# Performance work log

Measured on AMD Instinct MI355X. Metric: run time of the kernel, lower is better.

The kernel has to match this reference:

```python
import jax, jax.numpy as jnp
import numpy as np

N_NODES = 100000
N_EDGES = 800000
NODE_F = 32
EDGE_F = 16
HID = 128
EPS = 1e-5


def _bn(h, g, b):
    # BatchNorm1d in training mode: biased batch stats over dim 0
    m = h.mean(axis=0)
    v = jnp.mean((h - m) ** 2, axis=0)
    return (h - m) * jax.lax.rsqrt(v + EPS) * g + b


def _sage(x, src, dst, Wl, bl, Wr):
    # PyG SAGEConv (mean aggr): lin_l(mean_{j->i} x_j) + lin_r(x_i)
    s = jax.ops.segment_sum(x[src], dst, num_segments=N_NODES)
    cnt = jax.ops.segment_sum(jnp.ones((src.shape[0], 1), x.dtype), dst, num_segments=N_NODES)
    mean = s / jnp.maximum(cnt, 1.0)
    return mean @ Wl + bl + x @ Wr


def setup_inputs() -> dict:
    key = jax.random.key(0)
    ks = jax.random.split(key, 32)

    def lin(k, fi, fo):
        return jax.random.normal(k, (fi, fo), jnp.float32) / np.sqrt(fi)

    inp = {
        'x': jax.random.normal(ks[0], (N_NODES, NODE_F), jnp.float32),
        'edge_index': jax.random.randint(ks[1], (2, N_EDGES), 0, N_NODES),
        'edge_attr': jax.random.normal(ks[2], (N_EDGES, EDGE_F), jnp.float32),
        'edge_source': jax.random.randint(ks[3], (N_EDGES,), 0, N_NODES),
        'edge_target': jax.random.randint(ks[4], (N_EDGES,), 0, N_NODES),
        'W1l': lin(ks[5], NODE_F, HID), 'b1': jnp.zeros((HID,), jnp.float32), 'W1r': lin(ks[6], NODE_F, HID),
        'W2l': lin(ks[7], HID, HID), 'b2': jnp.zeros((HID,), jnp.float32), 'W2r': lin(ks[8], HID, HID),
        'bn1_g': jnp.ones((HID,), jnp.float32), 'bn1_b': jnp.zeros((HID,), jnp.float32),
        'bn2_g': jnp.ones((HID,), jnp.float32), 'bn2_b': jnp.zeros((HID,), jnp.float32),
        'We': lin(ks[9], EDGE_F, HID), 'be': jnp.zeros((HID,), jnp.float32),
        'bne_g': jnp.ones((HID,), jnp.float32), 'bne_b': jnp.zeros((HID,), jnp.float32),
        'Wm1': lin(ks[10], 3 * HID, HID), 'bm1': jnp.zeros((HID,), jnp.float32),
        'bnm_g': jnp.ones((HID,), jnp.float32), 'bnm_b': jnp.zeros((HID,), jnp.float32),
        'Wm2': lin(ks[11], HID, HID // 2), 'bm2': jnp.zeros((HID // 2,), jnp.float32),
        'Wm3': lin(ks[12], HID // 2, 1), 'bm3': jnp.zeros((1,), jnp.float32),
    }
    return inp


def reference(x, edge_index, edge_attr, edge_source, edge_target,
              W1l, b1, W1r, W2l, b2, W2r, bn1_g, bn1_b, bn2_g, bn2_b,
              We, be, bne_g, bne_b, Wm1, bm1, bnm_g, bnm_b, Wm2, bm2, Wm3, bm3):
    src, dst = edge_index[0], edge_index[1]
    h = jax.nn.relu(_bn(_sage(x, src, dst, W1l, b1, W1r), bn1_g, bn1_b))  # dropout = identity (eval)
    h = jax.nn.relu(_bn(_sage(h, src, dst, W2l, b2, W2r), bn2_g, bn2_b))
    ef = _bn(jax.nn.relu(edge_attr @ We + be), bne_g, bne_b)  # Linear->ReLU->BN->Dropout(id)
    z = jnp.concatenate([h[edge_source], h[edge_target], ef], axis=1)  # [E, 3*HID]
    z = _bn(jax.nn.relu(z @ Wm1 + bm1), bnm_g, bnm_b)
    z = jax.nn.relu(z @ Wm2 + bm2)
    return (z @ Wm3 + bm3).squeeze(-1)
```

## Files before the change

kernel.cpp:

```cpp
#include <hip/hip_runtime.h>
#include <hip/hip_bf16.h>

#define NN 100000
#define NE 800000
#define SCAN_NB 98

typedef __attribute__((ext_vector_type(8))) short bf16x8;
typedef __attribute__((ext_vector_type(4))) float f32x4;

__device__ __forceinline__ short f2b(float f) {
    unsigned u = __float_as_uint(f);
    unsigned r = (u + 0x7fffu + ((u >> 16) & 1u)) >> 16;
    return (short)r;
}
__device__ __forceinline__ float b2f(short s) {
    return __uint_as_float(((unsigned)(unsigned short)s) << 16);
}

__global__ __launch_bounds__(256) void k_prep_hist(
    const float* __restrict__ We, const float* __restrict__ Wm1,
    const float* __restrict__ W2l, const float* __restrict__ W2r,
    short* __restrict__ WteT, short* __restrict__ WmsT,
    short* __restrict__ WmdT, short* __restrict__ W2cT,
    const int* __restrict__ ei, int* __restrict__ deg)
{
    int b = blockIdx.x;
    int tid = threadIdx.x;
    if (b >= 5) {
        int e = (b - 5) * 256 + tid;
        if (e < NE) atomicAdd(&deg[ei[NE + e]], 1);
        return;
    }
// ... 85 lines not shown
    }
    float s1[4] = {0,0,0,0}, s2[4] = {0,0,0,0};
    f32x4 zero = {0.f, 0.f, 0.f, 0.f};
    __syncthreads();

    const int G = gridDim.x - SCAT_NB;
    const int NT = NE / 32;
    float4 fe0 = {0,0,0,0}, fe1 = {0,0,0,0};
    int t = blockIdx.x - SCAT_NB;
    if (t < NT && quad < 2) {
        const float* p = ea + (size_t)(t * 32 + row16 + ln) * 16 + quad * 8;
        fe0 = *(const float4*)p; fe1 = *(const float4*)(p + 4);
    }
    for (; t < NT; t += G) {
        bf16x8 aE;
        #pragma unroll
        for (int i = 0; i < 8; i++) aE[i] = 0;
        if (quad < 2) {
            aE[0]=f2b(fe0.x); aE[1]=f2b(fe0.y); aE[2]=f2b(fe0.z); aE[3]=f2b(fe0.w);
            aE[4]=f2b(fe1.x); aE[5]=f2b(fe1.y); aE[6]=f2b(fe1.z); aE[7]=f2b(fe1.w);
        }
        int t1 = t + G;
        if (t1 < NT && quad < 2) {
            const float* p = ea + (size_t)(t1 * 32 + row16 + ln) * 16 + quad * 8;
            fe0 = *(const float4*)p; fe1 = *(const float4*)(p + 4);
        }
        f32x4 tacc[4];
        #pragma unroll
        for (int nt = 0; nt < 4; nt++)
            tacc[nt] = __builtin_amdgcn_mfma_f32_16x16x32_bf16(aE, bWe[nt], zero, 0, 0, 0);
        #pragma unroll
        for (int nt = 0; nt < 4; nt++)
            #pragma unroll
            for (int r = 0; r < 4; r++) {
                float v = fmaxf(tacc[nt][r] + bec[nt], 0.f);
// ... 73 lines not shown
    int c0 = (threadIdx.x & 31) * 4;
    float sc[4], sh[4];
    #pragma unroll
    for (int i = 0; i < 4; i++) {
        float m = ssum1[c0 + i] / (float)NN;
        float var = ssq1[c0 + i] / (float)NN - m * m;
        float rs = rsqrtf(var + 1e-5f);
        float s = g1[c0 + i] * rs;
        sc[i] = s; sh[i] = b1g[c0 + i] - m * s;
    }
    int b = rowptr[n], e = rowptr[n + 1];
    float acc[4] = {0.f, 0.f, 0.f, 0.f};
    int i = b;
    for (; i + 4 <= e; i += 4) {
        int s0 = elist[i], s1 = elist[i + 1], s2 = elist[i + 2], s3 = elist[i + 3];
        ushort4 u0 = *(const ushort4*)(h1b + (size_t)s0 * 128 + c0);
        ushort4 u1 = *(const ushort4*)(h1b + (size_t)s1 * 128 + c0);
        ushort4 u2 = *(const ushort4*)(h1b + (size_t)s2 * 128 + c0);
        ushort4 u3 = *(const ushort4*)(h1b + (size_t)s3 * 128 + c0);
        acc[0] += fmaxf(b2f((short)u0.x) * sc[0] + sh[0], 0.f) + fmaxf(b2f((short)u1.x) * sc[0] + sh[0], 0.f)
                + fmaxf(b2f((short)u2.x) * sc[0] + sh[0], 0.f) + fmaxf(b2f((short)u3.x) * sc[0] + sh[0], 0.f);
        acc[1] += fmaxf(b2f((short)u0.y) * sc[1] + sh[1], 0.f) + fmaxf(b2f((short)u1.y) * sc[1] + sh[1], 0.f)
                + fmaxf(b2f((short)u2.y) * sc[1] + sh[1], 0.f) + fmaxf(b2f((short)u3.y) * sc[1] + sh[1], 0.f);
        acc[2] += fmaxf(b2f((short)u0.z) * sc[2] + sh[2], 0.f) + fmaxf(b2f((short)u1.z) * sc[2] + sh[2], 0.f)
                + fmaxf(b2f((short)u2.z) * sc[2] + sh[2], 0.f) + fmaxf(b2f((short)u3.z) * sc[2] + sh[2], 0.f);
        acc[3] += fmaxf(b2f((short)u0.w) * sc[3] + sh[3], 0.f) + fmaxf(b2f((short)u1.w) * sc[3] + sh[3], 0.f)
                + fmaxf(b2f((short)u2.w) * sc[3] + sh[3], 0.f) + fmaxf(b2f((short)u3.w) * sc[3] + sh[3], 0.f);
    }
    for (; i < e; i++) {
        int s = elist[i];
        ushort4 u = *(const ushort4*)(h1b + (size_t)s * 128 + c0);
        acc[0] += fmaxf(b2f((short)u.x) * sc[0] + sh[0], 0.f);
        acc[1] += fmaxf(b2f((short)u.y) * sc[1] + sh[1], 0.f);
        acc[2] += fmaxf(b2f((short)u.z) * sc[2] + sh[2], 0.f);
        acc[3] += fmaxf(b2f((short)u.w) * sc[3] + sh[3], 0.f);
    }
    float inv = (e > b) ? 1.0f / (float)(e - b) : 1.0f;
    ushort4 o;
    o.x = (unsigned short)f2b(acc[0] * inv);
    o.y = (unsigned short)f2b(acc[1] * inv);
    o.z = (unsigned short)f2b(acc[2] * inv);
    o.w = (unsigned short)f2b(acc[3] * inv);
    *(ushort4*)(m2b + (size_t)n * 128 + c0) = o;
}

__global__ __launch_bounds__(256) void k_node_l1(
    const float* __restrict__ meanX, const float* __restrict__ x,
    const float* __restrict__ Wl, const float* __restrict__ Wr,
    const float* __restrict__ bias,
    short* __restrict__ outp, float* __restrict__ ssum, float* __restrict__ ssq)
{
    __shared__ __align__(16) float sWl[32][128];
    __shared__ __align__(16) float sWr[32][128];
    __shared__ __align__(16) float sA[32][36];
    __shared__ __align__(16) float sB[32][36];
    __shared__ float red[2][128], red2[2][128];
    int tid = threadIdx.x;
    int j = tid & 127, rg = tid >> 7;
// ... 18 lines not shown
    for (int kq = 0; kq < 8; kq++) {
        int k = kq * 4;
        float wl0 = sWl[k][j], wl1 = sWl[k+1][j], wl2 = sWl[k+2][j], wl3 = sWl[k+3][j];
        float wr0 = sWr[k][j], wr1 = sWr[k+1][j], wr2 = sWr[k+2][j], wr3 = sWr[k+3][j];
        #pragma unroll
        for (int r = 0; r < 16; r++) {
            float4 a = *(float4*)(&sA[rb + r][k]);
            float4 b = *(float4*)(&sB[rb + r][k]);
            acc[r] += a.x*wl0 + a.y*wl1 + a.z*wl2 + a.w*wl3
                    + b.x*wr0 + b.y*wr1 + b.z*wr2 + b.w*wr3;
        }
    }
    float bj = bias[j];
    float s1 = 0.0f, s2 = 0.0f;
    #pragma unroll
    for (int r = 0; r < 16; r++) {
        float v = acc[r] + bj;
        outp[(size_t)(r0 + rb + r) * 128 + j] = f2b(v);
        s1 += v; s2 += v * v;
    }
    red[rg][j] = s1; red2[rg][j] = s2;
    __syncthreads();
    if (rg == 0) {
        atomicAdd(&ssum[j], red[0][j] + red[1][j]);
        atomicAdd(&ssq[j],  red2[0][j] + red2[1][j]);
    }
}

__global__ __launch_bounds__(256) void k_node_l2m(
    const short* __restrict__ m2b, const short* __restrict__ h1b,
    const float* __restrict__ ssum1, const float* __restrict__ ssq1,
    const float* __restrict__ g1, const float* __restrict__ b1g,
    const short* __restrict__ W2cT, const float* __restrict__ bias,
    short* __restrict__ h2b, float* __restrict__ ssum, float* __restrict__ ssq)
// ... 27 lines not shown
    float s1[4] = {0,0,0,0}, s2[4] = {0,0,0,0};
    f32x4 zero = {0.f, 0.f, 0.f, 0.f};
    __syncthreads();

    for (int t = blockIdx.x; t < NN / 32; t += gridDim.x) {
        int r0 = t * 32;
        __syncthreads();
        {
            int r = tid >> 3, seg = tid & 7;
            if (seg < 4) {
                const bf16x8* src = (const bf16x8*)(m2b + (size_t)(r0 + r) * 128 + seg * 32);
                bf16x8* dst = (bf16x8*)(&sK[r][seg * 32]);
                dst[0] = src[0]; dst[1] = src[1]; dst[2] = src[2]; dst[3] = src[3];
            } else {
                int c0 = (seg - 4) * 32;
                const short* src = h1b + (size_t)(r0 + r) * 128 + c0;
                short tmp[32];
                #pragma unroll
                for (int i = 0; i < 32; i++)
                    tmp[i] = f2b(fmaxf(b2f(src[i]) * sS[c0 + i] + sH[c0 + i], 0.f));
                bf16x8* dst = (bf16x8*)(&sK[r][128 + c0]);
                dst[0] = *(bf16x8*)(tmp); dst[1] = *(bf16x8*)(tmp + 8);
                dst[2] = *(bf16x8*)(tmp + 16); dst[3] = *(bf16x8*)(tmp + 24);
            }
        }
        __syncthreads();
        f32x4 acc[4] = {zero, zero, zero, zero};
        #pragma unroll
        for (int kk = 0; kk < 8; kk++) {
            bf16x8 a = *(const bf16x8*)(&sK[row16 + ln][kk * 32 + quad * 8]);
            #pragma unroll
            for (int nt = 0; nt < 4; nt++)
                acc[nt] = __builtin_amdgcn_mfma_f32_16x16x32_bf16(a, bW[nt][kk], acc[nt], 0, 0, 0);
        }
        #pragma unroll
        for (int nt = 0; nt < 4; nt++) {
            int col = colbase + nt * 16 + ln;
            #pragma unroll
            for (int r = 0; r < 4; r++) {
                float v = acc[nt][r] + bc[nt];
                h2b[(size_t)(r0 + row16 + quad * 4 + r) * 128 + col] = f2b(v);
                s1[nt] += v; s2[nt] += v * v;
            }
        }
    }
    #pragma unroll
    for (int nt = 0; nt < 4; nt++) {
        float a1 = s1[nt], a2 = s2[nt];
        a1 += __shfl_down(a1, 32); a1 += __shfl_down(a1, 16);
        a2 += __shfl_down(a2, 32); a2 += __shfl_down(a2, 16);
        if (quad == 0) {
            atomicAdd(&sRed[0][colbase + nt * 16 + ln], a1);
            atomicAdd(&sRed[1][colbase + nt * 16 + ln], a2);
        }
    }
    __syncthreads();
    if (tid < 128) {
        atomicAdd(&ssum[tid], sRed[0][tid]);
        atomicAdd(&ssq[tid],  sRed[1][tid]);
    }
}

__global__ void k_fold_m(const float* __restrict__ ssum, const float* __restrict__ ssq,
    const float* __restrict__ g, const float* __restrict__ b,
    const float* __restrict__ Wm2, const float* __restrict__ bm2,
    short* __restrict__ W2pT, float* __restrict__ b2p)
{
    __shared__ float sa[128], sc[128];
    int tid = threadIdx.x;
    float m = ssum[tid] / (float)NE;
    float var = ssq[tid] / (float)NE - m * m;
    float rs = rsqrtf(var + 1e-5f);
    float a = g[tid] * rs;
    sa[tid] = a; sc[tid] = b[tid] - m * a;
    __syncthreads();
    if (tid < 64) {
        float acc = bm2[tid];
        for (int k = 0; k < 128; k++) {
            float w = Wm2[k * 64 + tid];
            W2pT[tid * 128 + k] = f2b(sa[k] * w);
            acc += sc[k] * w;
        }
        b2p[tid] = acc;
    }
}

__global__ __launch_bounds__(256) void k_proj_mfma(
    const short* __restrict__ h2b,
    const float* __restrict__ ssum2, const float* __restrict__ ssq2,
    const float* __restrict__ g2, const float* __restrict__ b2g,
    const short* __restrict__ WT0, const short* __restrict__ WT1,
    short* __restrict__ C0, short* __restrict__ C1)
{
    __shared__ __align__(16) short sA[32][136];
    __shared__ float sS[128], sH[128];
    const int tid = threadIdx.x;
    const int wave = tid >> 6, lane = tid & 63, quad = lane >> 4, ln = lane & 15;
    const int waveM = wave >> 1, waveN = wave & 1;
// ... 10 lines not shown
        sS[tid] = s; sH[tid] = b2g[tid] - m * s;
    }
    bf16x8 bW[4][4];
    #pragma unroll
    for (int nt = 0; nt < 4; nt++)
        #pragma unroll
        for (int kk = 0; kk < 4; kk++)
            bW[nt][kk] = *(const bf16x8*)(WT + (colbase + nt * 16 + ln) * 128 + kk * 32 + quad * 8);
    f32x4 zero = {0.f, 0.f, 0.f, 0.f};
    __syncthreads();
    for (int t = b0; t < NN / 32; t += 512) {
        int r0 = t * 32;
        __syncthreads();
        {
            int r = tid >> 3, c0 = (tid & 7) * 16;
            const short* p = h2b + (size_t)(r0 + r) * 128 + c0;
            short tmp[16];
            #pragma unroll
            for (int i = 0; i < 16; i++)
                tmp[i] = f2b(fmaxf(b2f(p[i]) * sS[c0 + i] + sH[c0 + i], 0.f));
            *(bf16x8*)(&sA[r][c0])     = *(bf16x8*)tmp;
            *(bf16x8*)(&sA[r][c0 + 8]) = *(bf16x8*)(tmp + 8);
        }
        __syncthreads();
        f32x4 acc[4] = {zero, zero, zero, zero};
        #pragma unroll
        for (int kk = 0; kk < 4; kk++) {
            bf16x8 a = *(const bf16x8*)(&sA[row16 + ln][kk * 32 + quad * 8]);
            #pragma unroll
            for (int nt = 0; nt < 4; nt++)
                acc[nt] = __builtin_amdgcn_mfma_f32_16x16x32_bf16(a, bW[nt][kk], acc[nt], 0, 0, 0);
        }
        #pragma unroll
        for (int nt = 0; nt < 4; nt++) {
            int col = colbase + nt * 16 + ln;
            #pragma unroll
            for (int r = 0; r < 4; r++)
                C[(size_t)(r0 + row16 + quad * 4 + r) * 128 + col] = f2b(acc[nt][r]);
        }
    }
}

template<int MODE, bool STOREV = false>
__global__ __launch_bounds__(256) void k_edge_mfma(
    const float* __restrict__ ea,
    const short* __restrict__ WteT, const float* __restrict__ be,
    const short* __restrict__ W1pT, const float* __restrict__ bm1p,
    const short* __restrict__ hs, const short* __restrict__ hd,
    const int* __restrict__ esrc, const int* __restrict__ etgt,
    const short* __restrict__ W2pT, const float* __restrict__ b2p,
    const float* __restrict__ Wm3, const float* __restrict__ bm3,
    float* __restrict__ ssum, float* __restrict__ ssq,
    short* __restrict__ vbuf, float* __restrict__ outp)
{
    __shared__ __align__(16) short sT[32][136];
    __shared__ __align__(16) float sSum[32][132];
    __shared__ float sRed[2][128];
    __shared__ __align__(16) short sWe[128][16];
    __shared__ __align__(16) short sW2[64][136];
    __shared__ float sZ[32][69];
    __shared__ float sW3[64];

    const int tid = threadIdx.x;
    const int wave = tid >> 6, lane = tid & 63;
    const int quad = lane >> 4, ln = lane & 15;
    const int waveM = wave >> 1, waveN = wave & 1;
    const int colbase = 64 * waveN, row16 = 16 * waveM;

    if (MODE < 2) {
        if (tid < 128) { sRed[0][tid] = 0.f; sRed[1][tid] = 0.f; }
    }
    if (MODE <= 2) {
        int r = tid >> 1, cs = (tid & 1) * 8;
        *(bf16x8*)(&sWe[r][cs]) = *(const bf16x8*)(WteT + r * 32 + cs);
    }
    if (MODE >= 2) {
        int q = tid >> 2, kb = (tid & 3) * 32;
        const bf16x8* src = (const bf16x8*)(W2pT + q * 128 + kb);
        bf16x8* dst = (bf16x8*)(&sW2[q][kb]);
        dst[0] = src[0]; dst[1] = src[1]; dst[2] = src[2]; dst[3] = src[3];
        if (tid < 64) sW3[tid] = Wm3[tid];
    }

    bf16x8 bW1[4][4];
    if (MODE == 1 || MODE == 2) {
        #pragma unroll
        for (int nt = 0; nt < 4; nt++)
            #pragma unroll
            for (int kk = 0; kk < 4; kk++)
                bW1[nt][kk] = *(const bf16x8*)(W1pT + (colbase + nt * 16 + ln) * 128 + kk * 32 + quad * 8);
    }
    float bec[4], bmc[4];
    #pragma unroll
    for (int nt = 0; nt < 4; nt++) {
        bec[nt] = (MODE <= 2) ? be[colbase + nt * 16 + ln] : 0.f;
        bmc[nt] = (MODE == 1 || MODE == 2) ? bm1p[colbase + nt * 16 + ln] : 0.f;
    }
    float b2c[2] = {0.f, 0.f};
    if (MODE >= 2) { b2c[0] = b2p[32 * waveN + ln]; b2c[1] = b2p[32 * waveN + 16 + ln]; }
    float bm3v = (MODE >= 2) ? bm3[0] : 0.f;

    const int srow = tid >> 4;
    const int scol = (tid & 15) * 8;

    float s1[4] = {0,0,0,0}, s2[4] = {0,0,0,0};
    f32x4 zero = {0.f, 0.f, 0.f, 0.f};
    __syncthreads();

    if constexpr (MODE == 1) {
        const int G = gridDim.x;
        const int NT = NE / 32;
        bf16x8 gA = {}, gB = {}, gC = {}, gD = {};
        int i1sA = 0, i1tA = 0, i1sB = 0, i1tB = 0;
        float4 fe0 = {0,0,0,0}, fe1 = {0,0,0,0};
// ... 11 lines not shown
            if (t1 < NT) {
                const int e1 = t1 * 32;
                i1sA = esrc[e1 + srow];      i1tA = etgt[e1 + srow];
                i1sB = esrc[e1 + srow + 16]; i1tB = etgt[e1 + srow + 16];
            }
            if (quad < 2) {
                const float* p = ea + (size_t)(e0 + row16 + ln) * 16 + quad * 8;
                fe0 = *(const float4*)p; fe1 = *(const float4*)(p + 4);
            }
        }

        for (; t < NT; t += G) {
            const int e0 = t * 32;

            bf16x8 aE;
            #pragma unroll
            for (int i = 0; i < 8; i++) aE[i] = 0;
            if (quad < 2) {
                aE[0]=f2b(fe0.x); aE[1]=f2b(fe0.y); aE[2]=f2b(fe0.z); aE[3]=f2b(fe0.w);
                aE[4]=f2b(fe1.x); aE[5]=f2b(fe1.y); aE[6]=f2b(fe1.z); aE[7]=f2b(fe1.w);
            }
            f32x4 tacc[4];
            #pragma unroll
            for (int nt = 0; nt < 4; nt++) {
                bf16x8 bWe_ = *(const bf16x8*)(&sWe[colbase + nt * 16 + ln][(quad & 1) * 8]);
                tacc[nt] = __builtin_amdgcn_mfma_f32_16x16x32_bf16(aE, bWe_, zero, 0, 0, 0);
            }

            __syncthreads();

            #pragma unroll
            for (int nt = 0; nt < 4; nt++) {
                int col = colbase + nt * 16 + ln;
                #pragma unroll
                for (int r = 0; r < 4; r++)
                    sT[row16 + quad * 4 + r][col] = f2b(fmaxf(tacc[nt][r] + bec[nt], 0.f));
            }
            {
                f32x4 a0, a1, b0, b1;
                #pragma unroll
                for (int i = 0; i < 4; i++) {
                    a0[i] = b2f(gA[i])     + b2f(gB[i]);
                    a1[i] = b2f(gA[i + 4]) + b2f(gB[i + 4]);
                    b0[i] = b2f(gC[i])     + b2f(gD[i]);
                    b1[i] = b2f(gC[i + 4]) + b2f(gD[i + 4]);
                }
                *(f32x4*)(&sSum[srow][scol])          = a0;
                *(f32x4*)(&sSum[srow][scol + 4])      = a1;
                *(f32x4*)(&sSum[srow + 16][scol])     = b0;
                *(f32x4*)(&sSum[srow + 16][scol + 4]) = b1;
            }
            {
                int t1 = t + G;
                if (t1 < NT) {
                    gA = *(const bf16x8*)(hs + (size_t)i1sA * 128 + scol);
                    gB = *(const bf16x8*)(hd + (size_t)i1tA * 128 + scol);
                    gC = *(const bf16x8*)(hs + (size_t)i1sB * 128 + scol);
                    gD = *(const bf16x8*)(hd + (size_t)i1tB * 128 + scol);
                    int t2 = t1 + G;
                    if (t2 < NT) {
                        const int e2 = t2 * 32;
// ... 7 lines not shown
                }
            }
            __syncthreads();

            f32x4 uacc[4] = {zero, zero, zero, zero};
            #pragma unroll
            for (int kk = 0; kk < 4; kk++) {
                bf16x8 aU = *(const bf16x8*)(&sT[row16 + ln][kk * 32 + quad * 8]);
                #pragma unroll
                for (int nt = 0; nt < 4; nt++)
                    uacc[nt] = __builtin_amdgcn_mfma_f32_16x16x32_bf16(aU, bW1[nt][kk], uacc[nt], 0, 0, 0);
            }
            #pragma unroll
            for (int nt = 0; nt < 4; nt++) {
                int col = colbase + nt * 16 + ln;
                #pragma unroll
                for (int r = 0; r < 4; r++) {
                    float v = uacc[nt][r] + bmc[nt] + sSum[row16 + quad * 4 + r][col];
                    v = fmaxf(v, 0.f);
                    s1[nt] += v; s2[nt] += v * v;
                    if constexpr (STOREV)
                        vbuf[(size_t)(e0 + row16 + quad * 4 + r) * 128 + col] = f2b(v);
                }
            }
        }
    } else if constexpr (MODE == 3) {
        const int G = gridDim.x;
        const int NT = NE / 32;
        bf16x8 aV0 = {}, aV1 = {}, aV2 = {}, aV3 = {};
        int t = blockIdx.x;
        if (t < NT) {
            const short* p = vbuf + (size_t)(t * 32 + row16 + ln) * 128 + quad * 8;
            aV0 = *(const bf16x8*)(p);
            aV1 = *(const bf16x8*)(p + 32);
            aV2 = *(const bf16x8*)(p + 64);
            aV3 = *(const bf16x8*)(p + 96);
        }
// ... 31 lines not shown
            }
            __syncthreads();
            {
                int row = wave * 8 + (lane >> 3);
                int ks  = (lane & 7) * 8;
                float o = 0.f;
                #pragma unroll
                for (int k2 = 0; k2 < 8; k2++)
                    o += sZ[row][ks + k2] * sW3[ks + k2];
                o += __shfl_xor(o, 1);
                o += __shfl_xor(o, 2);
                o += __shfl_xor(o, 4);
                if ((lane & 7) == 0) outp[e0 + row] = o + bm3v;
            }
        }
    } else {
    for (int t = blockIdx.x; t < NE / 32; t += gridDim.x) {
        const int e0 = t * 32;

        int isA = esrc[e0 + srow],      itA = etgt[e0 + srow];
        int isB = esrc[e0 + srow + 16], itB = etgt[e0 + srow + 16];

        bf16x8 aE;
        #pragma unroll
        for (int i = 0; i < 8; i++) aE[i] = 0;
        if (quad < 2) {
            const float* p = ea + (size_t)(e0 + row16 + ln) * 16 + quad * 8;
            float4 f0 = *(const float4*)p, f1 = *(const float4*)(p + 4);
            aE[0]=f2b(f0.x); aE[1]=f2b(f0.y); aE[2]=f2b(f0.z); aE[3]=f2b(f0.w);
            aE[4]=f2b(f1.x); aE[5]=f2b(f1.y); aE[6]=f2b(f1.z); aE[7]=f2b(f1.w);
        }
        f32x4 tacc[4];
        #pragma unroll
        for (int nt = 0; nt < 4; nt++) {
            bf16x8 bWe_ = *(const bf16x8*)(&sWe[colbase + nt * 16 + ln][(quad & 1) * 8]);
            tacc[nt] = __builtin_amdgcn_mfma_f32_16x16x32_bf16(aE, bWe_, zero, 0, 0, 0);
        }

        __syncthreads();
        {
            bf16x8 gA = *(const bf16x8*)(hs + (size_t)isA * 128 + scol);
            bf16x8 gB = *(const bf16x8*)(hd + (size_t)itA * 128 + scol);
            bf16x8 gC = *(const bf16x8*)(hs + (size_t)isB * 128 + scol);
            bf16x8 gD = *(const bf16x8*)(hd + (size_t)itB * 128 + scol);
            #pragma unroll
            for (int nt = 0; nt < 4; nt++) {
                int col = colbase + nt * 16 + ln;
                #pragma unroll
                for (int r = 0; r < 4; r++)
                    sT[row16 + quad * 4 + r][col] = f2b(fmaxf(tacc[nt][r] + bec[nt], 0.f));
            }
            f32x4 a0, a1, b0, b1;
            #pragma unroll
            for (int i = 0; i < 4; i++) {
                a0[i] = b2f(gA[i])     + b2f(gB[i]);
                a1[i] = b2f(gA[i + 4]) + b2f(gB[i + 4]);
                b0[i] = b2f(gC[i])     + b2f(gD[i]);
                b1[i] = b2f(gC[i + 4]) + b2f(gD[i + 4]);
            }
            *(f32x4*)(&sSum[srow][scol])          = a0;
            *(f32x4*)(&sSum[srow][scol + 4])      = a1;
            *(f32x4*)(&sSum[srow + 16][scol])     = b0;
            *(f32x4*)(&sSum[srow + 16][scol + 4]) = b1;
        }
        __syncthreads();

        f32x4 uacc[4] = {zero, zero, zero, zero};
        #pragma unroll
        for (int kk = 0; kk < 4; kk++) {
            bf16x8 aU = *(const bf16x8*)(&sT[row16 + ln][kk * 32 + quad * 8]);
            #pragma unroll
            for (int nt = 0; nt < 4; nt++)
                uacc[nt] = __builtin_amdgcn_mfma_f32_16x16x32_bf16(aU, bW1[nt][kk], uacc[nt], 0, 0, 0);
        }
// ... 100 lines not shown
    float* bm1p  = (float*)A(512); float* b2p = (float*)A(256);
    short* WteT  = (short*)A(128 * 32 * 2);
    short* W1pT  = (short*)A(128 * 128 * 2);
    short* WmsT  = (short*)A(128 * 128 * 2);
    short* WmdT  = (short*)A(128 * 128 * 2);
    short* W2pT  = (short*)A(64 * 128 * 2);
    short* W2cT  = (short*)A(128 * 256 * 2);
    size_t chain = o;
    float* meanX = (float*)A((size_t)NN * 32 * 4);
    short* h1b   = (short*)A((size_t)NN * 128 * 2);
    short* m2b   = (short*)A((size_t)NN * 128 * 2);
    short* h2b   = (short*)A((size_t)NN * 128 * 2);
    int*   stmp  = (int*)meanX;
    short* vbuf  = (short*)(base + chain);
    bool storev = ws_size >= chain + (size_t)NE * 128 * 2;

    hipMemsetAsync(deg, 0, (size_t)NN * 4, stream);
    hipMemsetAsync(st, 0, 1024 * 4, stream);

    k_prep_hist<<<5 + (NE + 255) / 256, 256, 0, stream>>>(We, Wm1, W2l, W2r,
        WteT, WmsT, WmdT, W2cT, ei, deg);
    k_scan_a<<<SCAN_NB, 1024, 0, stream>>>(deg, stmp, bsum);
    k_scan_b<<<1, 64, 0, stream>>>(bsum, boff, rowptr);
    k_scan_c<<<SCAN_NB, 1024, 0, stream>>>(stmp, boff, rowptr, wp);

    k_scat_e0<<<SCAT_NB + 2048, 256, 0, stream>>>(ei, wp, elist,
        eattr, WteT, be, st + 512, st + 640);

    k_gagg1f<<<NN / 8 + 1, 256, 0, stream>>>(x, rowptr, elist, meanX,
        st + 512, st + 640, bne_g, bne_b, Wm1, bm1, W1pT, bm1p);
    k_node_l1<<<NN / 32, 256, 0, stream>>>(meanX, x, W1l, W1r, b1, h1b, st + 0, st + 128);

    k_gagg2<<<NN / 8, 256, 0, stream>>>(h1b, rowptr, elist, st + 0, st + 128, bn1_g, bn1_b, m2b);
    k_node_l2m<<<512, 256, 0, stream>>>(m2b, h1b, st + 0, st + 128, bn1_g, bn1_b,
        W2cT, b2, h2b, st + 256, st + 384);

    k_proj_mfma<<<1024, 256, 0, stream>>>(h2b, st + 256, st + 384, bn2_g, bn2_b,
        WmsT, WmdT, hsb, hdb);

    if (storev)
        k_edge_mfma<1, true><<<1280, 256, 0, stream>>>(eattr, WteT, be, W1pT, bm1p, hsb, hdb,
            esrc, etgt, W2pT, b2p, Wm3, bm3, st + 768, st + 896, vbuf, out);
    else
        k_edge_mfma<1, false><<<1280, 256, 0, stream>>>(eattr, WteT, be, W1pT, bm1p, hsb, hdb,
            esrc, etgt, W2pT, b2p, Wm3, bm3, st + 768, st + 896, nullptr, out);
    k_fold_m<<<1, 128, 0, stream>>>(st + 768, st + 896, bnm_g, bnm_b, Wm2, bm2, W2pT, b2p);

    if (storev)
        k_edge_mfma<3><<<1536, 256, 0, stream>>>(eattr, WteT, be, W1pT, bm1p, hsb, hdb,
            esrc, etgt, W2pT, b2p, Wm3, bm3, nullptr, nullptr, vbuf, out);
    else
        k_edge_mfma<2><<<1024, 256, 0, stream>>>(eattr, WteT, be, W1pT, bm1p, hsb, hdb,
            esrc, etgt, W2pT, b2p, Wm3, bm3, nullptr, nullptr, nullptr, out);
}
```

Measured before the change: 756.2 us.

## Use packed bf16 conversions, fold BN into edge kernels, keep We in registers

Replaces the scalar software float-to-bf16 rounding with the hardware v_cvt_pk_bf16_f32 pair instruction throughout. bf16 unpacking now uses 32-bit words with shift and mask. The separate k_fold_m launch is removed: each MODE>=2 edge block recomputes the BN-folded Wm2 and bias into shared memory. We weights are held in registers instead of shared memory, and the MODE-1 grid shrinks from 1280 to 1024 blocks. This cuts ALU work and one launch, at the cost of every block redoing the 128x64 fold.

```diff
diff --git a/kernel.cpp b/kernel.cpp
--- a/kernel.cpp
+++ b/kernel.cpp
@@ -16,6 +16,13 @@
 __device__ __forceinline__ float b2f(short s) {
     return __uint_as_float(((unsigned)(unsigned short)s) << 16);
 }
+__device__ __forceinline__ unsigned cvt2(float a, float b) {
+    unsigned r;
+    asm("v_cvt_pk_bf16_f32 %0, %1, %2" : "=v"(r) : "v"(a), "v"(b));
+    return r;
+}
+__device__ __forceinline__ float blo(unsigned u) { return __uint_as_float(u << 16); }
+__device__ __forceinline__ float bhi(unsigned u) { return __uint_as_float(u & 0xffff0000u); }
 
 __global__ __launch_bounds__(256) void k_prep_hist(
     const float* __restrict__ We, const float* __restrict__ Wm1,
@@ -131,11 +138,14 @@
     }
     for (; t < NT; t += G) {
         bf16x8 aE;
-        #pragma unroll
-        for (int i = 0; i < 8; i++) aE[i] = 0;
         if (quad < 2) {
-            aE[0]=f2b(fe0.x); aE[1]=f2b(fe0.y); aE[2]=f2b(fe0.z); aE[3]=f2b(fe0.w);
-            aE[4]=f2b(fe1.x); aE[5]=f2b(fe1.y); aE[6]=f2b(fe1.z); aE[7]=f2b(fe1.w);
+            uint4 uw;
+            uw.x = cvt2(fe0.x, fe0.y); uw.y = cvt2(fe0.z, fe0.w);
+            uw.z = cvt2(fe1.x, fe1.y); uw.w = cvt2(fe1.z, fe1.w);
+            aE = *(bf16x8*)&uw;
+        } else {
+            #pragma unroll
+            for (int i = 0; i < 8; i++) aE[i] = 0;
         }
         int t1 = t + G;
         if (t1 < NT && quad < 2) {
@@ -239,34 +249,32 @@
     int i = b;
     for (; i + 4 <= e; i += 4) {
         int s0 = elist[i], s1 = elist[i + 1], s2 = elist[i + 2], s3 = elist[i + 3];
-        ushort4 u0 = *(const ushort4*)(h1b + (size_t)s0 * 128 + c0);
-        ushort4 u1 = *(const ushort4*)(h1b + (size_t)s1 * 128 + c0);
-        ushort4 u2 = *(const ushort4*)(h1b + (size_t)s2 * 128 + c0);
-        ushort4 u3 = *(const ushort4*)(h1b + (size_t)s3 * 128 + c0);
-        acc[0] += fmaxf(b2f((short)u0.x) * sc[0] + sh[0], 0.f) + fmaxf(b2f((short)u1.x) * sc[0] + sh[0], 0.f)
-                + fmaxf(b2f((short)u2.x) * sc[0] + sh[0], 0.f) + fmaxf(b2f((short)u3.x) * sc[0] + sh[0], 0.f);
-        acc[1] += fmaxf(b2f((short)u0.y) * sc[1] + sh[1], 0.f) + fmaxf(b2f((short)u1.y) * sc[1] + sh[1], 0.f)
-                + fmaxf(b2f((short)u2.y) * sc[1] + sh[1], 0.f) + fmaxf(b2f((short)u3.y) * sc[1] + sh[1], 0.f);
-        acc[2] += fmaxf(b2f((short)u0.z) * sc[2] + sh[2], 0.f) + fmaxf(b2f((short)u1.z) * sc[2] + sh[2], 0.f)
-                + fmaxf(b2f((short)u2.z) * sc[2] + sh[2], 0.f) + fmaxf(b2f((short)u3.z) * sc[2] + sh[2], 0.f);
-        acc[3] += fmaxf(b2f((short)u0.w) * sc[3] + sh[3], 0.f) + fmaxf(b2f((short)u1.w) * sc[3] + sh[3], 0.f)
-                + fmaxf(b2f((short)u2.w) * sc[3] + sh[3], 0.f) + fmaxf(b2f((short)u3.w) * sc[3] + sh[3], 0.f);
+        uint2 u0 = *(const uint2*)(h1b + (size_t)s0 * 128 + c0);
+        uint2 u1 = *(const uint2*)(h1b + (size_t)s1 * 128 + c0);
+        uint2 u2 = *(const uint2*)(h1b + (size_t)s2 * 128 + c0);
+        uint2 u3 = *(const uint2*)(h1b + (size_t)s3 * 128 + c0);
+        acc[0] += fmaxf(blo(u0.x) * sc[0] + sh[0], 0.f) + fmaxf(blo(u1.x) * sc[0] + sh[0], 0.f)
+                + fmaxf(blo(u2.x) * sc[0] + sh[0], 0.f) + fmaxf(blo(u3.x) * sc[0] + sh[0], 0.f);
+        acc[1] += fmaxf(bhi(u0.x) * sc[1] + sh[1], 0.f) + fmaxf(bhi(u1.x) * sc[1] + sh[1], 0.f)
+                + fmaxf(bhi(u2.x) * sc[1] + sh[1], 0.f) + fmaxf(bhi(u3.x) * sc[1] + sh[1], 0.f);
+        acc[2] += fmaxf(blo(u0.y) * sc[2] + sh[2], 0.f) + fmaxf(blo(u1.y) * sc[2] + sh[2], 0.f)
+                + fmaxf(blo(u2.y) * sc[2] + sh[2], 0.f) + fmaxf(blo(u3.y) * sc[2] + sh[2], 0.f);
+        acc[3] += fmaxf(bhi(u0.y) * sc[3] + sh[3], 0.f) + fmaxf(bhi(u1.y) * sc[3] + sh[3], 0.f)
+                + fmaxf(bhi(u2.y) * sc[3] + sh[3], 0.f) + fmaxf(bhi(u3.y) * sc[3] + sh[3], 0.f);
     }
     for (; i < e; i++) {
         int s = elist[i];
-        ushort4 u = *(const ushort4*)(h1b + (size_t)s * 128 + c0);
-        acc[0] += fmaxf(b2f((short)u.x) * sc[0] + sh[0], 0.f);
-        acc[1] += fmaxf(b2f((short)u.y) * sc[1] + sh[1], 0.f);
-        acc[2] += fmaxf(b2f((short)u.z) * sc[2] + sh[2], 0.f);
-        acc[3] += fmaxf(b2f((short)u.w) * sc[3] + sh[3], 0.f);
+        uint2 u = *(const uint2*)(h1b + (size_t)s * 128 + c0);
+        acc[0] += fmaxf(blo(u.x) * sc[0] + sh[0], 0.f);
+        acc[1] += fmaxf(bhi(u.x) * sc[1] + sh[1], 0.f);
+        acc[2] += fmaxf(blo(u.y) * sc[2] + sh[2], 0.f);
+        acc[3] += fmaxf(bhi(u.y) * sc[3] + sh[3], 0.f);
     }
     float inv = (e > b) ? 1.0f / (float)(e - b) : 1.0f;
-    ushort4 o;
-    o.x = (unsigned short)f2b(acc[0] * inv);
-    o.y = (unsigned short)f2b(acc[1] * inv);
-    o.z = (unsigned short)f2b(acc[2] * inv);
-    o.w = (unsigned short)f2b(acc[3] * inv);
-    *(ushort4*)(m2b + (size_t)n * 128 + c0) = o;
+    uint2 ow;
+    ow.x = cvt2(acc[0] * inv, acc[1] * inv);
+    ow.y = cvt2(acc[2] * inv, acc[3] * inv);
+    *(uint2*)(m2b + (size_t)n * 128 + c0) = ow;
 }
 
 __global__ __launch_bounds__(256) void k_node_l1(
@@ -315,10 +323,12 @@
     float bj = bias[j];
     float s1 = 0.0f, s2 = 0.0f;
     #pragma unroll
-    for (int r = 0; r < 16; r++) {
-        float v = acc[r] + bj;
-        outp[(size_t)(r0 + rb + r) * 128 + j] = f2b(v);
-        s1 += v; s2 += v * v;
+    for (int r = 0; r < 16; r += 2) {
+        float v0 = acc[r] + bj, v1 = acc[r + 1] + bj;
+        s1 += v0 + v1; s2 += v0 * v0 + v1 * v1;
+        unsigned p = cvt2(v0, v1);
+        outp[(size_t)(r0 + rb + r) * 128 + j]     = (short)p;
+        outp[(size_t)(r0 + rb + r + 1) * 128 + j] = (short)(p >> 16);
     }
     red[rg][j] = s1; red2[rg][j] = s2;
     __syncthreads();
@@ -376,14 +386,19 @@
                 dst[0] = src[0]; dst[1] = src[1]; dst[2] = src[2]; dst[3] = src[3];
             } else {
                 int c0 = (seg - 4) * 32;
-                const short* src = h1b + (size_t)(r0 + r) * 128 + c0;
-                short tmp[32];
+                const uint4* pw = (const uint4*)(h1b + (size_t)(r0 + r) * 128 + c0);
+                uint4* dw = (uint4*)(&sK[r][128 + c0]);
                 #pragma unroll
-                for (int i = 0; i < 32; i++)
-                    tmp[i] = f2b(fmaxf(b2f(src[i]) * sS[c0 + i] + sH[c0 + i], 0.f));
-                bf16x8* dst = (bf16x8*)(&sK[r][128 + c0]);
-                dst[0] = *(bf16x8*)(tmp); dst[1] = *(bf16x8*)(tmp + 8);
-                dst[2] = *(bf16x8*)(tmp + 16); dst[3] = *(bf16x8*)(tmp + 24);
+                for (int i2 = 0; i2 < 4; i2++) {
+                    uint4 u = pw[i2];
+                    int cb = c0 + i2 * 8;
+                    uint4 ow;
+                    ow.x = cvt2(fmaxf(blo(u.x)*sS[cb+0]+sH[cb+0],0.f), fmaxf(bhi(u.x)*sS[cb+1]+sH[cb+1],0.f));
+                    ow.y = cvt2(fmaxf(blo(u.y)*sS[cb+2]+sH[cb+2],0.f), fmaxf(bhi(u.y)*sS[cb+3]+sH[cb+3],0.f));
+                    ow.z = cvt2(fmaxf(blo(u.z)*sS[cb+4]+sH[cb+4],0.f), fmaxf(bhi(u.z)*sS[cb+5]+sH[cb+5],0.f));
+                    ow.w = cvt2(fmaxf(blo(u.w)*sS[cb+6]+sH[cb+6],0.f), fmaxf(bhi(u.w)*sS[cb+7]+sH[cb+7],0.f));
+                    dw[i2] = ow;
+                }
             }
         }
         __syncthreads();
@@ -398,12 +413,15 @@
         #pragma unroll
         for (int nt = 0; nt < 4; nt++) {
             int col = colbase + nt * 16 + ln;
-            #pragma unroll
-            for (int r = 0; r < 4; r++) {
-                float v = acc[nt][r] + bc[nt];
-                h2b[(size_t)(r0 + row16 + quad * 4 + r) * 128 + col] = f2b(v);
-                s1[nt] += v; s2[nt] += v * v;
-            }
+            float v0 = acc[nt][0] + bc[nt], v1 = acc[nt][1] + bc[nt];
+            float v2 = acc[nt][2] + bc[nt], v3 = acc[nt][3] + bc[nt];
+            s1[nt] += (v0 + v1) + (v2 + v3);
+            s2[nt] += (v0*v0 + v1*v1) + (v2*v2 + v3*v3);
+            unsigned p01 = cvt2(v0, v1), p23 = cvt2(v2, v3);
+            h2b[(size_t)(r0 + row16 + quad * 4 + 0) * 128 + col] = (short)p01;
+            h2b[(size_t)(r0 + row16 + quad * 4 + 1) * 128 + col] = (short)(p01 >> 16);
+            h2b[(size_t)(r0 + row16 + quad * 4 + 2) * 128 + col] = (short)p23;
+            h2b[(size_t)(r0 + row16 + quad * 4 + 3) * 128 + col] = (short)(p23 >> 16);
         }
     }
     #pragma unroll
@@ -420,30 +438,6 @@
     if (tid < 128) {
         atomicAdd(&ssum[tid], sRed[0][tid]);
         atomicAdd(&ssq[tid],  sRed[1][tid]);
-    }
-}
-
-__global__ void k_fold_m(const float* __restrict__ ssum, const float* __restrict__ ssq,
-    const float* __restrict__ g, const float* __restrict__ b,
-    const float* __restrict__ Wm2, const float* __restrict__ bm2,
-    short* __restrict__ W2pT, float* __restrict__ b2p)
-{
-    __shared__ float sa[128], sc[128];
-    int tid = threadIdx.x;
-    float m = ssum[tid] / (float)NE;
-    float var = ssq[tid] / (float)NE - m * m;
-    float rs = rsqrtf(var + 1e-5f);
-    float a = g[tid] * rs;
-    sa[tid] = a; sc[tid] = b[tid] - m * a;
-    __syncthreads();
-    if (tid < 64) {
-        float acc = bm2[tid];
-        for (int k = 0; k < 128; k++) {
-            float w = Wm2[k * 64 + tid];
-            W2pT[tid * 128 + k] = f2b(sa[k] * w);
-            acc += sc[k] * w;
-        }
-        b2p[tid] = acc;
     }
 }
 
@@ -484,13 +478,19 @@
         __syncthreads();
         {
             int r = tid >> 3, c0 = (tid & 7) * 16;
-            const short* p = h2b + (size_t)(r0 + r) * 128 + c0;
-            short tmp[16];
-            #pragma unroll
-            for (int i = 0; i < 16; i++)
-                tmp[i] = f2b(fmaxf(b2f(p[i]) * sS[c0 + i] + sH[c0 + i], 0.f));
-            *(bf16x8*)(&sA[r][c0])     = *(bf16x8*)tmp;
-            *(bf16x8*)(&sA[r][c0 + 8]) = *(bf16x8*)(tmp + 8);
+            const uint4* pw = (const uint4*)(h2b + (size_t)(r0 + r) * 128 + c0);
+            uint4* dw = (uint4*)(&sA[r][c0]);
+            #pragma unroll
+            for (int i2 = 0; i2 < 2; i2++) {
+                uint4 u = pw[i2];
+                int cb = c0 + i2 * 8;
+                uint4 ow;
+                ow.x = cvt2(fmaxf(blo(u.x)*sS[cb+0]+sH[cb+0],0.f), fmaxf(bhi(u.x)*sS[cb+1]+sH[cb+1],0.f));
+                ow.y = cvt2(fmaxf(blo(u.y)*sS[cb+2]+sH[cb+2],0.f), fmaxf(bhi(u.y)*sS[cb+3]+sH[cb+3],0.f));
+                ow.z = cvt2(fmaxf(blo(u.z)*sS[cb+4]+sH[cb+4],0.f), fmaxf(bhi(u.z)*sS[cb+5]+sH[cb+5],0.f));
+                ow.w = cvt2(fmaxf(blo(u.w)*sS[cb+6]+sH[cb+6],0.f), fmaxf(bhi(u.w)*sS[cb+7]+sH[cb+7],0.f));
+                dw[i2] = ow;
+            }
         }
         __syncthreads();
         f32x4 acc[4] = {zero, zero, zero, zero};
@@ -504,9 +504,12 @@
         #pragma unroll
         for (int nt = 0; nt < 4; nt++) {
             int col = colbase + nt * 16 + ln;
-            #pragma unroll
-            for (int r = 0; r < 4; r++)
-                C[(size_t)(r0 + row16 + quad * 4 + r) * 128 + col] = f2b(acc[nt][r]);
+            unsigned p01 = cvt2(acc[nt][0], acc[nt][1]);
+            unsigned p23 = cvt2(acc[nt][2], acc[nt][3]);
+            C[(size_t)(r0 + row16 + quad * 4 + 0) * 128 + col] = (short)p01;
+            C[(size_t)(r0 + row16 + quad * 4 + 1) * 128 + col] = (short)(p01 >> 16);
+            C[(size_t)(r0 + row16 + quad * 4 + 2) * 128 + col] = (short)p23;
+            C[(size_t)(r0 + row16 + quad * 4 + 3) * 128 + col] = (short)(p23 >> 16);
         }
     }
 }
@@ -518,7 +521,8 @@
     const short* __restrict__ W1pT, const float* __restrict__ bm1p,
     const short* __restrict__ hs, const short* __restrict__ hd,
     const int* __restrict__ esrc, const int* __restrict__ etgt,
-    const short* __restrict__ W2pT, const float* __restrict__ b2p,
+    const float* __restrict__ Wm2, const float* __restrict__ bm2,
+    const float* __restrict__ bnm_g, const float* __restrict__ bnm_b,
     const float* __restrict__ Wm3, const float* __restrict__ bm3,
     float* __restrict__ ssum, float* __restrict__ ssq,
     short* __restrict__ vbuf, float* __restrict__ outp)
@@ -526,7 +530,6 @@
     __shared__ __align__(16) short sT[32][136];
     __shared__ __align__(16) float sSum[32][132];
     __shared__ float sRed[2][128];
-    __shared__ __align__(16) short sWe[128][16];
     __shared__ __align__(16) short sW2[64][136];
     __shared__ float sZ[32][69];
     __shared__ float sW3[64];
@@ -540,25 +543,51 @@
     if (MODE < 2) {
         if (tid < 128) { sRed[0][tid] = 0.f; sRed[1][tid] = 0.f; }
     }
+    float b2c[2] = {0.f, 0.f};
+    if (MODE >= 2) {
+        float* sSc   = (float*)sZ;
+        float* sSh   = sSc + 128;
+        float* sPart = sSh + 128;
+        float* sB2   = sPart + 256;
+        if (tid < 128) {
+            float m = ssum[tid] / (float)NE;
+            float var = ssq[tid] / (float)NE - m * m;
+            float rs = rsqrtf(var + 1e-5f);
+            float a = bnm_g[tid] * rs;
+            sSc[tid] = a; sSh[tid] = bnm_b[tid] - m * a;
+        }
+        if (tid < 64) sW3[tid] = Wm3[tid];
+        __syncthreads();
+        {
+            int col = tid & 63, kg = tid >> 6;
+            float acc = 0.f;
+            for (int k = kg * 32; k < kg * 32 + 32; k++) {
+                float w = Wm2[k * 64 + col];
+                sW2[col][k] = f2b(sSc[k] * w);
+                acc += sSh[k] * w;
+            }
+            sPart[kg * 64 + col] = acc;
+        }
+        __syncthreads();
+        if (tid < 64)
+            ((float*)sZ)[512 + tid] = bm2[tid] + sPart[tid] + sPart[64 + tid]
+                                    + sPart[128 + tid] + sPart[192 + tid];
+        __syncthreads();
+        b2c[0] = sB2[32 * waveN + ln];
+        b2c[1] = sB2[32 * waveN + 16 + ln];
+    }
+
+    bf16x8 bWe[4], bW1[4][4];
     if (MODE <= 2) {
-        int r = tid >> 1, cs = (tid & 1) * 8;
-        *(bf16x8*)(&sWe[r][cs]) = *(const bf16x8*)(WteT + r * 32 + cs);
-    }
-    if (MODE >= 2) {
-        int q = tid >> 2, kb = (tid & 3) * 32;
-        const bf16x8* src = (const bf16x8*)(W2pT + q * 128 + kb);
-        bf16x8* dst = (bf16x8*)(&sW2[q][kb]);
-        dst[0] = src[0]; dst[1] = src[1]; dst[2] = src[2]; dst[3] = src[3];
-        if (tid < 64) sW3[tid] = Wm3[tid];
-    }
-
-    bf16x8 bW1[4][4];
-    if (MODE == 1 || MODE == 2) {
-        #pragma unroll
-        for (int nt = 0; nt < 4; nt++)
-            #pragma unroll
-            for (int kk = 0; kk < 4; kk++)
-                bW1[nt][kk] = *(const bf16x8*)(W1pT + (colbase + nt * 16 + ln) * 128 + kk * 32 + quad * 8);
+        #pragma unroll
+        for (int nt = 0; nt < 4; nt++) {
+            bWe[nt] = *(const bf16x8*)(WteT + (colbase + nt * 16 + ln) * 32 + quad * 8);
+            if (MODE >= 1) {
+                #pragma unroll
+                for (int kk = 0; kk < 4; kk++)
+                    bW1[nt][kk] = *(const bf16x8*)(W1pT + (colbase + nt * 16 + ln) * 128 + kk * 32 + quad * 8);
+            }
+        }
     }
     float bec[4], bmc[4];
     #pragma unroll
@@ -566,8 +595,6 @@
         bec[nt] = (MODE <= 2) ? be[colbase + nt * 16 + ln] : 0.f;
         bmc[nt] = (MODE == 1 || MODE == 2) ? bm1p[colbase + nt * 16 + ln] : 0.f;
     }
-    float b2c[2] = {0.f, 0.f};
-    if (MODE >= 2) { b2c[0] = b2p[32 * waveN + ln]; b2c[1] = b2p[32 * waveN + 16 + ln]; }
     float bm3v = (MODE >= 2) ? bm3[0] : 0.f;
 
     const int srow = tid >> 4;
@@ -609,37 +636,44 @@
             const int e0 = t * 32;
 
             bf16x8 aE;
-            #pragma unroll
-            for (int i = 0; i < 8; i++) aE[i] = 0;
             if (quad < 2) {
-                aE[0]=f2b(fe0.x); aE[1]=f2b(fe0.y); aE[2]=f2b(fe0.z); aE[3]=f2b(fe0.w);
-                aE[4]=f2b(fe1.x); aE[5]=f2b(fe1.y); aE[6]=f2b(fe1.z); aE[7]=f2b(fe1.w);
+                uint4 uw;
+                uw.x = cvt2(fe0.x, fe0.y); uw.y = cvt2(fe0.z, fe0.w);
+                uw.z = cvt2(fe1.x, fe1.y); uw.w = cvt2(fe1.z, fe1.w);
+                aE = *(bf16x8*)&uw;
+            } else {
+                #pragma unroll
+                for (int i = 0; i < 8; i++) aE[i] = 0;
             }
             f32x4 tacc[4];
             #pragma unroll
-            for (int nt = 0; nt < 4; nt++) {
-                bf16x8 bWe_ = *(const bf16x8*)(&sWe[colbase + nt * 16 + ln][(quad & 1) * 8]);
-                tacc[nt] = __builtin_amdgcn_mfma_f32_16x16x32_bf16(aE, bWe_, zero, 0, 0, 0);
-            }
+            for (int nt = 0; nt < 4; nt++)
+                tacc[nt] = __builtin_amdgcn_mfma_f32_16x16x32_bf16(aE, bWe[nt], zero, 0, 0, 0);
 
             __syncthreads();
 
             #pragma unroll
             for (int nt = 0; nt < 4; nt++) {
                 int col = colbase + nt * 16 + ln;
-                #pragma unroll
-                for (int r = 0; r < 4; r++)
-                    sT[row16 + quad * 4 + r][col] = f2b(fmaxf(tacc[nt][r] + bec[nt], 0.f));
+                unsigned p01 = cvt2(fmaxf(tacc[nt][0] + bec[nt], 0.f), fmaxf(tacc[nt][1] + bec[nt], 0.f));
+                unsigned p23 = cvt2(fmaxf(tacc[nt][2] + bec[nt], 0.f), fmaxf(tacc[nt][3] + bec[nt], 0.f));
+                sT[row16 + quad * 4 + 0][col] = (short)p01;
+                sT[row16 + quad * 4 + 1][col] = (short)(p01 >> 16);
+                sT[row16 + quad * 4 + 2][col] = (short)p23;
+                sT[row16 + quad * 4 + 3][col] = (short)(p23 >> 16);
             }
             {
+                uint4 uA = *(const uint4*)&gA, uB = *(const uint4*)&gB;
+                uint4 uC = *(const uint4*)&gC, uD = *(const uint4*)&gD;
                 f32x4 a0, a1, b0, b1;
-                #pragma unroll
-                for (int i = 0; i < 4; i++) {
-                    a0[i] = b2f(gA[i])     + b2f(gB[i]);
-                    a1[i] = b2f(gA[i + 4]) + b2f(gB[i + 4]);
-                    b0[i] = b2f(gC[i])     + b2f(gD[i]);
-                    b1[i] = b2f(gC[i + 4]) + b2f(gD[i + 4]);
-                }
+                a0[0] = blo(uA.x) + blo(uB.x); a0[1] = bhi(uA.x) + bhi(uB.x);
+                a0[2] = blo(uA.y) + blo(uB.y); a0[3] = bhi(uA.y) + bhi(uB.y);
+                a1[0] = blo(uA.z) + blo(uB.z); a1[1] = bhi(uA.z) + bhi(uB.z);
+                a1[2] = blo(uA.w) + blo(uB.w); a1[3] = bhi(uA.w) + bhi(uB.w);
+                b0[0] = blo(uC.x) + blo(uD.x); b0[1] = bhi(uC.x) + bhi(uD.x);
+                b0[2] = blo(uC.y) + blo(uD.y); b0[3] = bhi(uC.y) + bhi(uD.y);
+                b1[0] = blo(uC.z) + blo(uD.z); b1[1] = bhi(uC.z) + bhi(uD.z);
+                b1[2] = blo(uC.w) + blo(uD.w); b1[3] = bhi(uC.w) + bhi(uD.w);
                 *(f32x4*)(&sSum[srow][scol])          = a0;
                 *(f32x4*)(&sSum[srow][scol + 4])      = a1;
                 *(f32x4*)(&sSum[srow + 16][scol])     = b0;
@@ -677,13 +711,18 @@
             #pragma unroll
             for (int nt = 0; nt < 4; nt++) {
                 int col = colbase + nt * 16 + ln;
-                #pragma unroll
-                for (int r = 0; r < 4; r++) {
-                    float v = uacc[nt][r] + bmc[nt] + sSum[row16 + quad * 4 + r][col];
-                    v = fmaxf(v, 0.f);
-                    s1[nt] += v; s2[nt] += v * v;
-                    if constexpr (STOREV)
-                        vbuf[(size_t)(e0 + row16 + quad * 4 + r) * 128 + col] = f2b(v);
+                float v0 = fmaxf(uacc[nt][0] + bmc[nt] + sSum[row16 + quad * 4 + 0][col], 0.f);
+                float v1 = fmaxf(uacc[nt][1] + bmc[nt] + sSum[row16 + quad * 4 + 1][col], 0.f);
+                float v2 = fmaxf(uacc[nt][2] + bmc[nt] + sSum[row16 + quad * 4 + 2][col], 0.f);
+                float v3 = fmaxf(uacc[nt][3] + bmc[nt] + sSum[row16 + quad * 4 + 3][col], 0.f);
+                s1[nt] += (v0 + v1) + (v2 + v3);
+                s2[nt] += (v0*v0 + v1*v1) + (v2*v2 + v3*v3);
+                if constexpr (STOREV) {
+                    unsigned p01 = cvt2(v0, v1), p23 = cvt2(v2, v3);
+                    vbuf[(size_t)(e0 + row16 + quad * 4 + 0) * 128 + col] = (short)p01;
+                    vbuf[(size_t)(e0 + row16 + quad * 4 + 1) * 128 + col] = (short)(p01 >> 16);
+                    vbuf[(size_t)(e0 + row16 + quad * 4 + 2) * 128 + col] = (short)p23;
+                    vbuf[(size_t)(e0 + row16 + quad * 4 + 3) * 128 + col] = (short)(p23 >> 16);
                 }
             }
         }
@@ -745,7 +784,7 @@
                 if ((lane & 7) == 0) outp[e0 + row] = o + bm3v;
             }
         }
-    } else {
+    } else if constexpr (MODE == 2) {
     for (int t = blockIdx.x; t < NE / 32; t += gridDim.x) {
         const int e0 = t * 32;
 
@@ -753,20 +792,21 @@
         int isB = esrc[e0 + srow + 16], itB = etgt[e0 + srow + 16];
 
         bf16x8 aE;
-        #pragma unroll
-        for (int i = 0; i < 8; i++) aE[i] = 0;
         if (quad < 2) {
             const float* p = ea + (size_t)(e0 + row16 + ln) * 16 + quad * 8;
             float4 f0 = *(const float4*)p, f1 = *(const float4*)(p + 4);
-            aE[0]=f2b(f0.x); aE[1]=f2b(f0.y); aE[2]=f2b(f0.z); aE[3]=f2b(f0.w);
-            aE[4]=f2b(f1.x); aE[5]=f2b(f1.y); aE[6]=f2b(f1.z); aE[7]=f2b(f1.w);
+            uint4 uw;
+            uw.x = cvt2(f0.x, f0.y); uw.y = cvt2(f0.z, f0.w);
+            uw.z = cvt2(f1.x, f1.y); uw.w = cvt2(f1.z, f1.w);
+            aE = *(bf16x8*)&uw;
+        } else {
+            #pragma unroll
+            for (int i = 0; i < 8; i++) aE[i] = 0;
         }
         f32x4 tacc[4];
         #pragma unroll
-        for (int nt = 0; nt < 4; nt++) {
-            bf16x8 bWe_ = *(const bf16x8*)(&sWe[colbase + nt * 16 + ln][(quad & 1) * 8]);
-            tacc[nt] = __builtin_amdgcn_mfma_f32_16x16x32_bf16(aE, bWe_, zero, 0, 0, 0);
-        }
+        for (int nt = 0; nt < 4; nt++)
+            tacc[nt] = __builtin_amdgcn_mfma_f32_16x16x32_bf16(aE, bWe[nt], zero, 0, 0, 0);
 
         __syncthreads();
         {
@@ -777,18 +817,24 @@
             #pragma unroll
             for (int nt = 0; nt < 4; nt++) {
                 int col = colbase + nt * 16 + ln;
-                #pragma unroll
-                for (int r = 0; r < 4; r++)
-                    sT[row16 + quad * 4 + r][col] = f2b(fmaxf(tacc[nt][r] + bec[nt], 0.f));
-            }
+                unsigned p01 = cvt2(fmaxf(tacc[nt][0] + bec[nt], 0.f), fmaxf(tacc[nt][1] + bec[nt], 0.f));
+                unsigned p23 = cvt2(fmaxf(tacc[nt][2] + bec[nt], 0.f), fmaxf(tacc[nt][3] + bec[nt], 0.f));
+                sT[row16 + quad * 4 + 0][col] = (short)p01;
+                sT[row16 + quad * 4 + 1][col] = (short)(p01 >> 16);
+                sT[row16 + quad * 4 + 2][col] = (short)p23;
+                sT[row16 + quad * 4 + 3][col] = (short)(p23 >> 16);
+            }
+            uint4 uA = *(const uint4*)&gA, uB = *(const uint4*)&gB;
+            uint4 uC = *(const uint4*)&gC, uD = *(const uint4*)&gD;
             f32x4 a0, a1, b0, b1;
-            #pragma unroll
-            for (int i = 0; i < 4; i++) {
-                a0[i] = b2f(gA[i])     + b2f(gB[i]);
-                a1[i] = b2f(gA[i + 4]) + b2f(gB[i + 4]);
-                b0[i] = b2f(gC[i])     + b2f(gD[i]);
-                b1[i] = b2f(gC[i + 4]) + b2f(gD[i + 4]);
-            }
+            a0[0] = blo(uA.x) + blo(uB.x); a0[1] = bhi(uA.x) + bhi(uB.x);
+            a0[2] = blo(uA.y) + blo(uB.y); a0[3] = bhi(uA.y) + bhi(uB.y);
+            a1[0] = blo(uA.z) + blo(uB.z); a1[1] = bhi(uA.z) + bhi(uB.z);
+            a1[2] = blo(uA.w) + blo(uB.w); a1[3] = bhi(uA.w) + bhi(uB.w);
+            b0[0] = blo(uC.x) + blo(uD.x); b0[1] = bhi(uC.x) + bhi(uD.x);
+            b0[2] = blo(uC.y) + blo(uD.y); b0[3] = bhi(uC.y) + bhi(uD.y);
+            b1[0] = blo(uC.z) + blo(uD.z); b1[1] = bhi(uC.z) + bhi(uD.z);
+            b1[2] = blo(uC.w) + blo(uD.w); b1[3] = bhi(uC.w) + bhi(uD.w);
             *(f32x4*)(&sSum[srow][scol])          = a0;
             *(f32x4*)(&sSum[srow][scol + 4])      = a1;
             *(f32x4*)(&sSum[srow + 16][scol])     = b0;
@@ -919,6 +965,7 @@
     int*   stmp  = (int*)meanX;
     short* vbuf  = (short*)(base + chain);
     bool storev = ws_size >= chain + (size_t)NE * 128 * 2;
+    (void)W2pT; (void)b2p; (void)sc1; (void)sh1; (void)sc2; (void)sh2;
 
     hipMemsetAsync(deg, 0, (size_t)NN * 4, stream);
     hipMemsetAsync(st, 0, 1024 * 4, stream);
@@ -944,17 +991,16 @@
         WmsT, WmdT, hsb, hdb);
 
     if (storev)
-        k_edge_mfma<1, true><<<1280, 256, 0, stream>>>(eattr, WteT, be, W1pT, bm1p, hsb, hdb,
-            esrc, etgt, W2pT, b2p, Wm3, bm3, st + 768, st + 896, vbuf, out);
+        k_edge_mfma<1, true><<<1024, 256, 0, stream>>>(eattr, WteT, be, W1pT, bm1p, hsb, hdb,
+            esrc, etgt, Wm2, bm2, bnm_g, bnm_b, Wm3, bm3, st + 768, st + 896, vbuf, out);
     else
-        k_edge_mfma<1, false><<<1280, 256, 0, stream>>>(eattr, WteT, be, W1pT, bm1p, hsb, hdb,
-            esrc, etgt, W2pT, b2p, Wm3, bm3, st + 768, st + 896, nullptr, out);
-    k_fold_m<<<1, 128, 0, stream>>>(st + 768, st + 896, bnm_g, bnm_b, Wm2, bm2, W2pT, b2p);
+        k_edge_mfma<1, false><<<1024, 256, 0, stream>>>(eattr, WteT, be, W1pT, bm1p, hsb, hdb,
+            esrc, etgt, Wm2, bm2, bnm_g, bnm_b, Wm3, bm3, st + 768, st + 896, nullptr, out);
 
     if (storev)
         k_edge_mfma<3><<<1536, 256, 0, stream>>>(eattr, WteT, be, W1pT, bm1p, hsb, hdb,
-            esrc, etgt, W2pT, b2p, Wm3, bm3, nullptr, nullptr, vbuf, out);
+            esrc, etgt, Wm2, bm2, bnm_g, bnm_b, Wm3, bm3, st + 768, st + 896, vbuf, out);
     else
         k_edge_mfma<2><<<1024, 256, 0, stream>>>(eattr, WteT, be, W1pT, bm1p, hsb, hdb,
-            esrc, etgt, W2pT, b2p, Wm3, bm3, nullptr, nullptr, nullptr, out);
-}
+            esrc, etgt, Wm2, bm2, bnm_g, bnm_b, Wm3, bm3, st + 768, st + 896, nullptr, out);
+}
```

After: 713.9 us. 5.6% less time.
